# Optimization experiments

Hardware: AMD Instinct MI355X
Metric: run time of the kernel (lower is better)

Reference implementation:

```python
import jax, jax.numpy as jnp
import numpy as np

DIM = 2048
N_HEAD = 16
HEAD_DIM = DIM // N_HEAD


def setup_inputs() -> dict:
    key = jax.random.key(0)
    k1, k2, k3 = jax.random.split(key, 3)
    B, N = 8, 4096
    x = jax.random.normal(k1, (B, N, DIM), dtype=jnp.float32)
    # torch nn.Linear weights: [out_features, in_features]
    w_qkv = jax.random.normal(k2, (3 * DIM, DIM), dtype=jnp.float32) * (DIM ** -0.5)
    w_proj = jax.random.normal(k3, (DIM, DIM), dtype=jnp.float32) * (DIM ** -0.5)
    return {"x": x, "w_qkv": w_qkv, "w_proj": w_proj}


def reference(x, w_qkv, w_proj):
    # Faithful to the original torch code, INCLUDING its layout quirk:
    # q,k,v stay [B, N, H, hd]; attention matrix is [B, N, H, H]
    # (softmax over heads, per token), matching q @ k.transpose(-2, -1).
    B, N, D = x.shape
    H, hd = N_HEAD, HEAD_DIM
    qkv = (x @ w_qkv.T).reshape(B, N, 3, H, hd)
    q, k, v = qkv[:, :, 0], qkv[:, :, 1], qkv[:, :, 2]  # each [B, N, H, hd]
    scale = hd ** -0.5
    att = jnp.einsum("bnid,bnjd->bnij", q, k) * scale  # [B, N, H, H]
    att = jax.nn.softmax(att, axis=-1)
    out = jnp.einsum("bnij,bnjd->bnid", att, v)  # [B, N, H, hd]
    # torch: .transpose(1, 2).reshape(B, N, D)
    out = out.transpose(0, 2, 1, 3).reshape(B, N, D)
    return out @ w_proj.T
```

## Files before the change

kernel.cpp:

```cpp
#include <hip/hip_runtime.h>


typedef unsigned short u16;
typedef unsigned int   u32;
typedef __bf16  bf16x8  __attribute__((ext_vector_type(8)));
typedef float   floatx4 __attribute__((ext_vector_type(4)));

#define GAS __attribute__((address_space(1)))
#define LAS __attribute__((address_space(3)))

__device__ __forceinline__ u16 f2bf(float x) {
  u32 u = __builtin_bit_cast(u32, x);
  return (u16)((u + 0x7FFFu + ((u >> 16) & 1u)) >> 16);
}
__device__ __forceinline__ u32 f2bf2(float lo, float hi) {
  u32 a = __builtin_bit_cast(u32, lo);
  u32 b = __builtin_bit_cast(u32, hi);
  a = (a + 0x7FFFu + ((a >> 16) & 1u)) >> 16;
  b = (b + 0x7FFFu + ((b >> 16) & 1u)) >> 16;
  return a | (b << 16);
}
__device__ __forceinline__ float bf2f(u32 lo16) {
  return __builtin_bit_cast(float, lo16 << 16);
}
__device__ __forceinline__ void unpack8(uint4 r, float* f) {
  f[0] = bf2f(r.x & 0xffffu); f[1] = bf2f(r.x >> 16);
  f[2] = bf2f(r.y & 0xffffu); f[3] = bf2f(r.y >> 16);
  f[4] = bf2f(r.z & 0xffffu); f[5] = bf2f(r.z >> 16);
  f[6] = bf2f(r.w & 0xffffu); f[7] = bf2f(r.w >> 16);
}

__global__ __launch_bounds__(256)
void cast_bf16_k(const float4* __restrict__ in, uint4* __restrict__ out, long n8) {
  long i = (long)blockIdx.x * 256 + threadIdx.x;
  if (i >= n8) return;
  float4 a = in[2 * i], b = in[2 * i + 1];
  uint4 o;
  o.x = f2bf2(a.x, a.y); o.y = f2bf2(a.z, a.w);
  o.z = f2bf2(b.x, b.y); o.w = f2bf2(b.z, b.w);
  out[i] = o;
}


__device__ __forceinline__ void mfma_16(floatx4 (&acc)[8][4], const bf16x8 (&a)[4],
                                        const bf16x8 (&b)[4], int ib) {
#pragma unroll
  for (int i = 0; i < 4; ++i)
#pragma unroll
    for (int n = 0; n < 4; ++n)
      acc[ib + i][n] = __builtin_amdgcn_mfma_f32_16x16x32_bf16(
          a[i], b[n], acc[ib + i][n], 0, 0, 0);
}

template<int OUT_BF16>
__global__ __launch_bounds__(512, 2)
void gemm256_k(const u16* __restrict__ A, const u16* __restrict__ B,
               void* __restrict__ Cv, int N_, int K, int nbx)
{
  __shared__ __align__(16) char smem[131072];

  const int nwg = (int)gridDim.x;
  const int id  = (int)blockIdx.x;
  const int swz = (id & 7) * (nwg >> 3) + (id >> 3);
  const int bx = swz % nbx, by = swz / nbx;
  const long tileM = (long)by << 8, tileN = (long)bx << 8;

  const int t = (int)threadIdx.x;
  const int wave = t >> 6, lane = t & 63;
  const int wm = wave >> 2, wn = wave & 3;
  const int lrow = lane & 15, lkq = lane >> 4;

  const int o0   = t << 4;
  const int r0   = (o0 >> 6) & 15;
  const int c0   = (o0 & 63) ^ ((r0 & 8) << 2);
  const int row0 = ((o0 >> 11) << 4) | r0;
  const int col0 = (((o0 >> 10) & 1) << 5) + (c0 >> 1);

  const u16* pA = A + (tileM + row0) * (long)K + col0;
  const u16* pB = B + (tileN + row0) * (long)K + col0;
  const long rs64 = (long)K << 6;
  const int  nkt  = K >> 6;

  const int innerF = (lrow << 6) | ((lkq << 4) ^ ((lrow & 8) << 2));
  const int aB = (wm << 14) + innerF;
  const int bB = 32768 + (wn << 13) + innerF;

  floatx4 acc[8][4] = {};
  bf16x8 af[2][4], bv[2][4];

  auto stage = [&](int s, int j) {
    const int base = ((j & 1) << 16) + ((s < 2) ? 32768 : 0) + ((s & 1) << 14) + (wave << 10);
    const u16* src = (s < 2) ? pB : pA;
    const long gofs = (long)(s & 1) * 2 * rs64 + ((long)j << 6);
    __builtin_amdgcn_global_load_lds((GAS void*)(src + gofs),        (LAS void*)(smem + base),        16, 0, 0);
    __builtin_amdgcn_global_load_lds((GAS void*)(src + gofs + rs64), (LAS void*)(smem + base + 8192), 16, 0, 0);
  };

  stage(0, 0); stage(1, 0); stage(2, 0); stage(3, 0);
  if (nkt > 1) { stage(0, 1); stage(1, 1); }
  if (nkt > 1) { asm volatile("s_waitcnt vmcnt(4)" ::: "memory"); }
  else         { asm volatile("s_waitcnt vmcnt(0)" ::: "memory"); }
  __builtin_amdgcn_s_barrier();
  __builtin_amdgcn_sched_barrier(0);

  for (int j = 0; j < nkt; ++j) {
    const int bufo = (j & 1) << 16;

    {
#pragma unroll
      for (int n = 0; n < 4; ++n)
        bv[0][n] = *(const bf16x8*)(smem + bufo + bB + (n << 11));
#pragma unroll
      for (int i = 0; i < 4; ++i)
        af[0][i] = *(const bf16x8*)(smem + bufo + aB + (i << 11));
      if (j + 1 < nkt) { stage(2, j + 1); stage(3, j + 1); }
      __builtin_amdgcn_s_barrier();
      asm volatile("s_waitcnt lgkmcnt(0)" ::: "memory");
      __builtin_amdgcn_sched_barrier(0);
      __builtin_amdgcn_s_setprio(1);
      mfma_16(acc, af[0], bv[0], 0);
      __builtin_amdgcn_s_setprio(0);
      __builtin_amdgcn_s_barrier();
      __builtin_amdgcn_sched_barrier(0);
    }
    {
#pragma unroll
      for (int n = 0; n < 4; ++n)
        bv[1][n] = *(const bf16x8*)(smem + bufo + bB + (n << 11) + 1024);
#pragma unroll
      for (int i = 0; i < 4; ++i)
        af[1][i] = *(const bf16x8*)(smem + bufo + aB + (i << 11) + 1024);
      __builtin_amdgcn_s_barrier();
      asm volatile("s_waitcnt lgkmcnt(0)" ::: "memory");
      __builtin_amdgcn_sched_barrier(0);
      __builtin_amdgcn_s_setprio(1);
      mfma_16(acc, af[1], bv[1], 0);
      __builtin_amdgcn_s_setprio(0);
      __builtin_amdgcn_s_barrier();
      __builtin_amdgcn_sched_barrier(0);
    }
    {
#pragma unroll
      for (int i = 0; i < 4; ++i)
        af[0][i] = *(const bf16x8*)(smem + bufo + aB + ((4 + i) << 11));
      if (j + 2 < nkt) { stage(0, j + 2); stage(1, j + 2); }
      __builtin_amdgcn_s_barrier();
      asm volatile("s_waitcnt lgkmcnt(0)" ::: "memory");
      __builtin_amdgcn_sched_barrier(0);
      __builtin_amdgcn_s_setprio(1);
      mfma_16(acc, af[0], bv[0], 4);
      __builtin_amdgcn_s_setprio(0);
      __builtin_amdgcn_s_barrier();
      __builtin_amdgcn_sched_barrier(0);
    }
    {
#pragma unroll
      for (int i = 0; i < 4; ++i)
        af[1][i] = *(const bf16x8*)(smem + bufo + aB + ((4 + i) << 11) + 1024);
      __builtin_amdgcn_s_barrier();
      asm volatile("s_waitcnt lgkmcnt(0)" ::: "memory");
      __builtin_amdgcn_sched_barrier(0);
      __builtin_amdgcn_s_setprio(1);
      mfma_16(acc, af[1], bv[1], 4);
      __builtin_amdgcn_s_setprio(0);
      if (j < nkt - 2)       { asm volatile("s_waitcnt vmcnt(4)" ::: "memory"); }
      else                   { asm volatile("s_waitcnt vmcnt(0)" ::: "memory"); }
      __builtin_amdgcn_s_barrier();
      __builtin_amdgcn_sched_barrier(0);
    }
  }

#pragma unroll
  for (int i = 0; i < 8; ++i) {
#pragma unroll
    for (int r = 0; r < 4; ++r) {
      const long row = tileM + wm * 128 + i * 16 + lkq * 4 + r;
#pragma unroll
      for (int n = 0; n < 4; ++n) {
        const long col = tileN + wn * 64 + n * 16 + lrow;
        const float v = acc[i][n][r];
        if (OUT_BF16) ((u16*)Cv)[row * (long)N_ + col] = f2bf(v);
        else          ((float*)Cv)[row * (long)N_ + col] = v;
      }
    }
  }
}

__global__ __launch_bounds__(256)
void attn_k(const u16* __restrict__ qkv, u16* __restrict__ y)
{
  __shared__ float sq[16 * 132];
  __shared__ float skT[128 * 17];
  __shared__ float sv[16 * 128];
  __shared__ float sS[16 * 17];
  __shared__ float sP[16 * 17];

  const int t = threadIdx.x;
  const int token = blockIdx.x;
  const int n = token & 4095;
  const int b = token >> 12;
  const u16* base = qkv + (long)token * 6144;

  float f[8];
  {
    uint4 raw = *(const uint4*)(base + t * 8);
    unpack8(raw, f);
    float* dst = &sq[(t >> 4) * 132 + (t & 15) * 8];
    ((float4*)dst)[0] = make_float4(f[0], f[1], f[2], f[3]);
    ((float4*)dst)[1] = make_float4(f[4], f[5], f[6], f[7]);
  }
  {
    uint4 raw = *(const uint4*)(base + 2048 + t * 8);
    unpack8(raw, f);
    const int j = t >> 4;
    const int d0 = (t & 15) * 8;
#pragma unroll
    for (int e = 0; e < 8; ++e) skT[(d0 + e) * 17 + j] = f[e];
  }
  {
    uint4 raw = *(const uint4*)(base + 4096 + t * 8);
    unpack8(raw, f);
    float* dst = &sv[t * 8];
    ((float4*)dst)[0] = make_float4(f[0], f[1], f[2], f[3]);
    ((float4*)dst)[1] = make_float4(f[4], f[5], f[6], f[7]);
  }
  __syncthreads();

  {
    const int i = t >> 4, j = t & 15;
    const float* qi = &sq[i * 132];
    float s = 0.f;
#pragma unroll 16
    for (int d = 0; d < 128; ++d) s += qi[d] * skT[d * 17 + j];
    sS[i * 17 + j] = s * 0.08838834764831845f;
  }
  __syncthreads();

  {
    const int i = t >> 4, j = t & 15;
    float mx = -1e30f;
#pragma unroll
    for (int jj = 0; jj < 16; ++jj) mx = fmaxf(mx, sS[i * 17 + jj]);
    float sum = 0.f;
#pragma unroll
    for (int jj = 0; jj < 16; ++jj) sum += __expf(sS[i * 17 + jj] - mx);
    sP[i * 17 + j] = __expf(sS[i * 17 + j] - mx) / sum;
  }
  __syncthreads();

  {
    const int i = t & 15, dblk = t >> 4;
    float o[8] = {};
#pragma unroll
    for (int jj = 0; jj < 16; ++jj) {
      const float p = sP[i * 17 + jj];
      const float* vv = &sv[jj * 128 + dblk * 8];
#pragma unroll
      for (int e = 0; e < 8; ++e) o[e] += p * vv[e];
    }
    const long row  = (long)b * 4096 + i * 256 + (n >> 4);
    const long colb = (long)(n & 15) * 128 + dblk * 8;
    uint4 pk;
    pk.x = f2bf2(o[0], o[1]); pk.y = f2bf2(o[2], o[3]);
    pk.z = f2bf2(o[4], o[5]); pk.w = f2bf2(o[6], o[7]);
    *(uint4*)&y[row * 2048 + colb] = pk;
  }
}

extern "C" void kernel_launch(void* const* d_in, const int* in_sizes, int n_in,
                              void* d_out, int out_size, void* d_ws, size_t ws_size,
                              hipStream_t stream)
{
  const float* x      = (const float*)d_in[0];
  const float* w_qkv  = (const float*)d_in[1];
  const float* w_proj = (const float*)d_in[2];

  const long NX  = 67108864L;
  const long NWQ = 12582912L;
  const long NWP = 4194304L;
  const long NQKV = 32768L * 6144;
  const long NY   = 32768L * 2048;

  char* ws = (char*)d_ws;
  u16* xb   = (u16*)ws;  ws += NX * 2;
  u16* wqb  = (u16*)ws;  ws += NWQ * 2;
  u16* wpb  = (u16*)ws;  ws += NWP * 2;
  u16* qkvb = (u16*)ws;  ws += NQKV * 2;
  u16* yb   = (u16*)ws;  ws += NY * 2;
  if (ws_size < (size_t)704643072L) return;

  cast_bf16_k<<<dim3((u32)(NX  / 2048)), 256, 0, stream>>>((const float4*)x,      (uint4*)xb,  NX  / 8);
  cast_bf16_k<<<dim3((u32)(NWQ / 2048)), 256, 0, stream>>>((const float4*)w_qkv,  (uint4*)wqb, NWQ / 8);
  cast_bf16_k<<<dim3((u32)(NWP / 2048)), 256, 0, stream>>>((const float4*)w_proj, (uint4*)wpb, NWP / 8);

  gemm256_k<1><<<dim3(24 * 128), 512, 0, stream>>>(xb, wqb, (void*)qkvb, 6144, 2048, 24);

  attn_k<<<dim3(32768), 256, 0, stream>>>(qkvb, yb);

  gemm256_k<0><<<dim3(8 * 128), 512, 0, stream>>>(yb, wpb, d_out, 2048, 2048, 8);
}
```

Baseline: 1.542 ms.

## Software-pipeline LDS fragment reads one phase ahead of MFMA in GEMM loop

Restructures the GEMM main loop so each phase's LDS fragment loads are issued one phase before they are consumed, using ping-pong register sets (afP/afQ, bv0/bv1). The explicit lgkmcnt(0) waits are removed so LDS reads overlap with MFMA execution, the vmcnt wait is moved earlier, and the next tile's first fragments are prefetched from the other buffer. This hides LDS latency but raises register pressure and relies on compiler-inserted waits for correctness.

```diff
diff --git a/kernel.cpp b/kernel.cpp
--- a/kernel.cpp
+++ b/kernel.cpp
@@ -41,7 +41,6 @@
   out[i] = o;
 }
 
-
 __device__ __forceinline__ void mfma_16(floatx4 (&acc)[8][4], const bf16x8 (&a)[4],
                                         const bf16x8 (&b)[4], int ib) {
 #pragma unroll
@@ -86,7 +85,7 @@
   const int bB = 32768 + (wn << 13) + innerF;
 
   floatx4 acc[8][4] = {};
-  bf16x8 af[2][4], bv[2][4];
+  bf16x8 afP[4], afQ[4], bv0[4], bv1[4];
 
   auto stage = [&](int s, int j) {
     const int base = ((j & 1) << 16) + ((s < 2) ? 32768 : 0) + ((s & 1) << 14) + (wave << 10);
@@ -95,6 +94,16 @@
     __builtin_amdgcn_global_load_lds((GAS void*)(src + gofs),        (LAS void*)(smem + base),        16, 0, 0);
     __builtin_amdgcn_global_load_lds((GAS void*)(src + gofs + rs64), (LAS void*)(smem + base + 8192), 16, 0, 0);
   };
+  auto rdB = [&](bf16x8 (&dst)[4], int bufo, int kk) {
+#pragma unroll
+    for (int n = 0; n < 4; ++n)
+      dst[n] = *(const bf16x8*)(smem + bufo + bB + (n << 11) + (kk << 10));
+  };
+  auto rdA = [&](bf16x8 (&dst)[4], int bufo, int q, int kk) {
+#pragma unroll
+    for (int i = 0; i < 4; ++i)
+      dst[i] = *(const bf16x8*)(smem + bufo + aB + ((q * 4 + i) << 11) + (kk << 10));
+  };
 
   stage(0, 0); stage(1, 0); stage(2, 0); stage(3, 0);
   if (nkt > 1) { stage(0, 1); stage(1, 1); }
@@ -102,69 +111,59 @@
   else         { asm volatile("s_waitcnt vmcnt(0)" ::: "memory"); }
   __builtin_amdgcn_s_barrier();
   __builtin_amdgcn_sched_barrier(0);
+  rdB(bv0, 0, 0);
+  rdA(afP, 0, 0, 0);
+  __builtin_amdgcn_sched_barrier(0);
 
   for (int j = 0; j < nkt; ++j) {
-    const int bufo = (j & 1) << 16;
+    const int bufo  = (j & 1) << 16;
+    const int nbufo = bufo ^ (1 << 16);
 
     {
-#pragma unroll
-      for (int n = 0; n < 4; ++n)
-        bv[0][n] = *(const bf16x8*)(smem + bufo + bB + (n << 11));
-#pragma unroll
-      for (int i = 0; i < 4; ++i)
-        af[0][i] = *(const bf16x8*)(smem + bufo + aB + (i << 11));
+      rdB(bv1, bufo, 1);
+      rdA(afQ, bufo, 0, 1);
       if (j + 1 < nkt) { stage(2, j + 1); stage(3, j + 1); }
       __builtin_amdgcn_s_barrier();
-      asm volatile("s_waitcnt lgkmcnt(0)" ::: "memory");
       __builtin_amdgcn_sched_barrier(0);
       __builtin_amdgcn_s_setprio(1);
-      mfma_16(acc, af[0], bv[0], 0);
+      mfma_16(acc, afP, bv0, 0);
       __builtin_amdgcn_s_setprio(0);
       __builtin_amdgcn_s_barrier();
       __builtin_amdgcn_sched_barrier(0);
     }
     {
-#pragma unroll
-      for (int n = 0; n < 4; ++n)
-        bv[1][n] = *(const bf16x8*)(smem + bufo + bB + (n << 11) + 1024);
-#pragma unroll
-      for (int i = 0; i < 4; ++i)
-        af[1][i] = *(const bf16x8*)(smem + bufo + aB + (i << 11) + 1024);
-      __builtin_amdgcn_s_barrier();
-      asm volatile("s_waitcnt lgkmcnt(0)" ::: "memory");
+      rdA(afP, bufo, 1, 0);
+      __builtin_amdgcn_s_barrier();
       __builtin_amdgcn_sched_barrier(0);
       __builtin_amdgcn_s_setprio(1);
-      mfma_16(acc, af[1], bv[1], 0);
+      mfma_16(acc, afQ, bv1, 0);
       __builtin_amdgcn_s_setprio(0);
       __builtin_amdgcn_s_barrier();
       __builtin_amdgcn_sched_barrier(0);
     }
     {
-#pragma unroll
-      for (int i = 0; i < 4; ++i)
-        af[0][i] = *(const bf16x8*)(smem + bufo + aB + ((4 + i) << 11));
+      rdA(afQ, bufo, 1, 1);
       if (j + 2 < nkt) { stage(0, j + 2); stage(1, j + 2); }
-      __builtin_amdgcn_s_barrier();
-      asm volatile("s_waitcnt lgkmcnt(0)" ::: "memory");
+      if (j < nkt - 2)       { asm volatile("s_waitcnt vmcnt(4)" ::: "memory"); }
+      else if (j == nkt - 2) { asm volatile("s_waitcnt vmcnt(0)" ::: "memory"); }
+      __builtin_amdgcn_s_barrier();
       __builtin_amdgcn_sched_barrier(0);
       __builtin_amdgcn_s_setprio(1);
-      mfma_16(acc, af[0], bv[0], 4);
+      mfma_16(acc, afP, bv0, 4);
       __builtin_amdgcn_s_setprio(0);
       __builtin_amdgcn_s_barrier();
       __builtin_amdgcn_sched_barrier(0);
     }
     {
-#pragma unroll
-      for (int i = 0; i < 4; ++i)
-        af[1][i] = *(const bf16x8*)(smem + bufo + aB + ((4 + i) << 11) + 1024);
-      __builtin_amdgcn_s_barrier();
-      asm volatile("s_waitcnt lgkmcnt(0)" ::: "memory");
+      if (j + 1 < nkt) {
+        rdB(bv0, nbufo, 0);
+        rdA(afP, nbufo, 0, 0);
+      }
+      __builtin_amdgcn_s_barrier();
       __builtin_amdgcn_sched_barrier(0);
       __builtin_amdgcn_s_setprio(1);
-      mfma_16(acc, af[1], bv[1], 4);
+      mfma_16(acc, afQ, bv1, 4);
       __builtin_amdgcn_s_setprio(0);
-      if (j < nkt - 2)       { asm volatile("s_waitcnt vmcnt(4)" ::: "memory"); }
-      else                   { asm volatile("s_waitcnt vmcnt(0)" ::: "memory"); }
       __builtin_amdgcn_s_barrier();
       __builtin_amdgcn_sched_barrier(0);
     }
```

After: 1.609 ms. +4.4%, slower.
